# Kernel tuning notes

Hardware: AMD Instinct MI355X
Metric: run time of the kernel (lower is better)

The kernel has to match this reference:

```python
import jax, jax.numpy as jnp
import numpy as np

B, C, T_TEXT, T_FEAT = 32, 256, 512, 2048
DELTA = 0.1  # self.temperature


def setup_inputs() -> dict:
    key = jax.random.key(0)
    k1, k2 = jax.random.split(key)
    x = jax.random.normal(k1, (B, C, T_TEXT), dtype=jnp.float32)
    # token durations in frames, ~U[0, 8): avg ~4 frames/token -> T_FEAT ~ 2048
    w = jax.random.uniform(k2, (B, T_TEXT), dtype=jnp.float32) * 8.0
    x_mask = jnp.ones((B, T_TEXT), dtype=bool)
    y_mask = jnp.ones((B, T_FEAT), dtype=bool)
    return {"x": x, "w": w, "x_mask": x_mask, "y_mask": y_mask}


def reference(x, w, x_mask, y_mask):
    # Gaussian upsampling (arXiv 2010.04301) with fixed temperature DELTA.
    # x: (B, C, T_text), w: (B, T_text), x_mask: (B, T_text), y_mask: (B, T_feat)
    T_feats = y_mask.shape[-1]
    # frame time indices, zeroed where y_mask is False
    t = jnp.arange(T_feats, dtype=jnp.float32)[None, :] * y_mask.astype(jnp.float32)  # (B, T_feat)
    # Gaussian centers: cumulative duration minus half of own duration
    c = jnp.cumsum(w, axis=-1) - 0.5 * w  # (B, T_text)
    # energy: -delta * (t - c)^2  -> (B, T_feat, T_text)
    energy = -DELTA * (t[:, :, None] - c[:, None, :]) ** 2
    # mask out padded text tokens
    energy = jnp.where(x_mask[:, None, :], energy, -jnp.inf)
    p_attn = jax.nn.softmax(energy, axis=-1)  # (B, T_feat, T_text)
    # weighted sum over text tokens: (B, C, T_feat)
    out = jnp.einsum("btn,bcn->bct", p_attn, x)
    return out
```

## Files before the change

kernel.cpp:

```cpp
#include <hip/hip_runtime.h>
#include <hip/hip_bf16.h>

#define B_    32
#define C_    256
#define NT    512
#define TFEAT 2048
#define TT    32
#define UW    96
#define PRE   32
#define DELTA 0.1f
#define PSTR  104
#define TPB   4
#define NGRP  16

typedef __attribute__((ext_vector_type(4))) float f32x4;
typedef __attribute__((ext_vector_type(8))) unsigned short u16x8;
typedef __attribute__((ext_vector_type(8))) __bf16 bf16x8;

static __device__ inline unsigned short f2bfbits(float f) {
    __bf16 h = (__bf16)f;
    return __builtin_bit_cast(unsigned short, h);
}
static __device__ inline float bf2f(unsigned short h) {
    return __uint_as_float(((unsigned)h) << 16);
}

__global__ __launch_bounds__(256, 2) void fused_kernel(const float* __restrict__ x,
                                                       const float* __restrict__ w,
                                                       float* __restrict__ out) {
    __shared__ float cs[NT];
    __shared__ float wsum[8];
    __shared__ unsigned short Pt[2][TT][PSTR];
    __shared__ float Sinv[2][TT];
    __shared__ int sLO[TPB];

    int tid  = threadIdx.x;
    int bx   = blockIdx.x;
    int b    = bx & 31;
    int grp  = bx >> 5;
    int lane = tid & 63;
    int wv   = tid >> 6;

    float v0 = w[b * NT + tid];
    float v1 = w[b * NT + 256 + tid];
    float s0 = v0, s1 = v1;
#pragma unroll
    for (int off = 1; off < 64; off <<= 1) {
        float t0 = __shfl_up(s0, off);
        float t1 = __shfl_up(s1, off);
        if (lane >= off) { s0 += t0; s1 += t1; }
    }
    if (lane == 63) { wsum[wv] = s0; wsum[4 + wv] = s1; }
    __syncthreads();
    float pre0 = 0.f;
    float pre1 = wsum[0] + wsum[1] + wsum[2] + wsum[3];
#pragma unroll
    for (int i = 0; i < 4; ++i) if (i < wv) pre0 += wsum[i];
#pragma unroll
    for (int i = 0; i < 4; ++i) if (i < wv) pre1 += wsum[4 + i];
    cs[tid]       = pre0 + s0 - 0.5f * v0;
    cs[256 + tid] = pre1 + s1 - 0.5f * v1;
    __syncthreads();

    if (wv == 0) {
        int gid = lane >> 4;
        int k   = lane & 15;
        float ft = (float)((grp * TPB + gid) * TT);
        bool p = cs[32 * k + 31] < ft;
        unsigned long long m = __ballot(p);
        int K = __popcll((m >> (gid * 16)) & 0xFFFFull);
        int n;
        if (K >= 16) {
            n = NT;
        } else {
            int base = 32 * K;
            bool pa = cs[base + k] < ft;
            bool pb = cs[base + 16 + k] < ft;
            unsigned long long ma = __ballot(pa);
            unsigned long long mb = __ballot(pb);
            n = base + __popcll((ma >> (gid * 16)) & 0xFFFFull)
                     + __popcll((mb >> (gid * 16)) & 0xFFFFull);
        }
        if (k == 0) {
            int n1 = n < NT - 1 ? n : NT - 1;
            int n0 = n - 1 > 0 ? n - 1 : 0;
            int nstar = (fabsf(ft - cs[n0]) <= fabsf(ft - cs[n1])) ? n0 : n1;
            int L = (nstar - PRE) & ~3;
            if (L < 0) L = 0;
            if (L > NT - UW) L = NT - UW;
            sLO[gid] = L;
        }
    }
    __syncthreads();

    int g = tid >> 3, j = tid & 7;
    int arow = lane & 15, kg = lane >> 4;

    f32x4 areg[12][2];

    auto issue_A = [&](int it) {
        int LO = sLO[it];
        const float* xb = x + ((size_t)b * C_) * NT + LO + kg * 8;
#pragma unroll
        for (int m = 0; m < 4; ++m) {
            const float* xr = xb + (size_t)(wv * 64 + m * 16 + arow) * NT;
#pragma unroll
            for (int ks = 0; ks < 3; ++ks) {
                areg[m * 3 + ks][0] = *reinterpret_cast<const f32x4*>(xr + ks * 32);
                areg[m * 3 + ks][1] = *reinterpret_cast<const f32x4*>(xr + ks * 32 + 4);
            }
        }
    };

    auto softmax_tile = [&](int it, int bf) {
        int LO = sLO[it];
        float ft = (float)((grp * TPB + it) * TT + g);
        float e[12];
        float mx = -1e30f;
#pragma unroll
        for (int k = 0; k < 12; ++k) {
            float d = ft - cs[LO + j + 8 * k];
            e[k] = -DELTA * d * d;
            mx = fmaxf(mx, e[k]);
        }
        mx = fmaxf(mx, __shfl_xor(mx, 1));
        mx = fmaxf(mx, __shfl_xor(mx, 2));
        mx = fmaxf(mx, __shfl_xor(mx, 4));
        float sum = 0.f;
#pragma unroll
        for (int k = 0; k < 12; ++k) {
            unsigned short pbv = f2bfbits(__expf(e[k] - mx));
            sum += bf2f(pbv);
            Pt[bf][g][j + 8 * k] = pbv;
        }
        sum += __shfl_xor(sum, 1);
        sum += __shfl_xor(sum, 2);
        sum += __shfl_xor(sum, 4);
        if (j == 0) Sinv[bf][g] = 1.f / fmaxf(sum, 1e-30f);
    };

    issue_A(0);
    __builtin_amdgcn_sched_barrier(0);
    softmax_tile(0, 0);
    __syncthreads();

    for (int it = 0; it < TPB; ++it) {
        int bf = it & 1;

        bf16x8 bfrag[6];
#pragma unroll
        for (int nt2 = 0; nt2 < 2; ++nt2)
#pragma unroll
            for (int ks = 0; ks < 3; ++ks)
                bfrag[nt2 * 3 + ks] = __builtin_bit_cast(bf16x8,
                    *reinterpret_cast<const u16x8*>(
                        &Pt[bf][nt2 * 16 + arow][ks * 32 + kg * 8]));

        f32x4 acc[4][2];
#pragma unroll
        for (int m = 0; m < 4; ++m)
#pragma unroll
            for (int nt2 = 0; nt2 < 2; ++nt2)
                acc[m][nt2] = (f32x4){0.f, 0.f, 0.f, 0.f};

#pragma unroll
        for (int m = 0; m < 4; ++m) {
            bf16x8 af[3];
#pragma unroll
            for (int ks = 0; ks < 3; ++ks) {
                bf16x8 vv;
#pragma unroll
                for (int q = 0; q < 4; ++q) {
                    vv[q]     = (__bf16)areg[m * 3 + ks][0][q];
                    vv[q + 4] = (__bf16)areg[m * 3 + ks][1][q];
                }
                af[ks] = vv;
            }
#pragma unroll
            for (int nt2 = 0; nt2 < 2; ++nt2)
#pragma unroll
                for (int ks = 0; ks < 3; ++ks)
                    acc[m][nt2] = __builtin_amdgcn_mfma_f32_16x16x32_bf16(
                        af[ks], bfrag[nt2 * 3 + ks], acc[m][nt2], 0, 0, 0);
        }

        float si0 = Sinv[bf][arow];
        float si1 = Sinv[bf][16 + arow];

        if (it < TPB - 1) {
            issue_A(it + 1);
            __builtin_amdgcn_sched_barrier(0);
            softmax_tile(it + 1, bf ^ 1);
        }
        __syncthreads();

        int t0 = (grp * TPB + it) * TT;
        float* ob = out + ((size_t)b * C_) * TFEAT + t0;
        int orow = kg * 4;
#pragma unroll
        for (int m = 0; m < 4; ++m) {
            int c = wv * 64 + m * 16 + orow;
#pragma unroll
            for (int r = 0; r < 4; ++r) {
                __builtin_nontemporal_store(acc[m][0][r] * si0,
                    ob + (size_t)(c + r) * TFEAT + arow);
                __builtin_nontemporal_store(acc[m][1][r] * si1,
                    ob + (size_t)(c + r) * TFEAT + 16 + arow);
            }
        }
    }
}

extern "C" void kernel_launch(void* const* d_in, const int* in_sizes, int n_in,
                              void* d_out, int out_size, void* d_ws, size_t ws_size,
                              hipStream_t stream) {
    const float* x = (const float*)d_in[0];
    const float* w = (const float*)d_in[1];
    float* out = (float*)d_out;

    hipLaunchKernelGGL(fused_kernel, dim3(B_ * NGRP), dim3(256), 0, stream,
                       x, w, out);
}
```

Baseline: 35.81 us.

## Transpose output through LDS for vectorized stores and split work across more blocks

Swaps the MFMA operand order so each wave's accumulator tile can be scaled and transposed through a small LDS buffer, then written as coalesced 128-bit row stores. Previously each lane issued scalar nontemporal stores. It also halves the tiles per block and doubles the grid, removing the register prefetch of x and the double-buffered softmax pipeline. The goal is to cut store-transaction overhead on the large output write and raise parallelism. The cost is less overlap of loads with compute, an extra LDS round trip, and the loss of nontemporal store hints.

```diff
diff --git a/kernel.cpp b/kernel.cpp
--- a/kernel.cpp
+++ b/kernel.cpp
@@ -10,8 +10,9 @@
 #define PRE   32
 #define DELTA 0.1f
 #define PSTR  104
-#define TPB   4
-#define NGRP  16
+#define TPB   2
+#define NGRP  32
+#define TSTR  36
 
 typedef __attribute__((ext_vector_type(4))) float f32x4;
 typedef __attribute__((ext_vector_type(8))) unsigned short u16x8;
@@ -30,9 +31,10 @@
                                                        float* __restrict__ out) {
     __shared__ float cs[NT];
     __shared__ float wsum[8];
-    __shared__ unsigned short Pt[2][TT][PSTR];
-    __shared__ float Sinv[2][TT];
+    __shared__ unsigned short Pt[TT][PSTR];
+    __shared__ float Sinv[TT];
     __shared__ int sLO[TPB];
+    __shared__ float trans[4][16][TSTR];
 
     int tid  = threadIdx.x;
     int bx   = blockIdx.x;
@@ -65,149 +67,127 @@
     if (wv == 0) {
         int gid = lane >> 4;
         int k   = lane & 15;
-        float ft = (float)((grp * TPB + gid) * TT);
-        bool p = cs[32 * k + 31] < ft;
-        unsigned long long m = __ballot(p);
-        int K = __popcll((m >> (gid * 16)) & 0xFFFFull);
-        int n;
-        if (K >= 16) {
-            n = NT;
-        } else {
-            int base = 32 * K;
-            bool pa = cs[base + k] < ft;
-            bool pb = cs[base + 16 + k] < ft;
-            unsigned long long ma = __ballot(pa);
-            unsigned long long mb = __ballot(pb);
-            n = base + __popcll((ma >> (gid * 16)) & 0xFFFFull)
-                     + __popcll((mb >> (gid * 16)) & 0xFFFFull);
-        }
-        if (k == 0) {
-            int n1 = n < NT - 1 ? n : NT - 1;
-            int n0 = n - 1 > 0 ? n - 1 : 0;
-            int nstar = (fabsf(ft - cs[n0]) <= fabsf(ft - cs[n1])) ? n0 : n1;
-            int L = (nstar - PRE) & ~3;
-            if (L < 0) L = 0;
-            if (L > NT - UW) L = NT - UW;
-            sLO[gid] = L;
+        if (gid < TPB) {
+            float ft = (float)((grp * TPB + gid) * TT);
+            bool p = cs[32 * k + 31] < ft;
+            unsigned long long m = __ballot(p);
+            int K = __popcll((m >> (gid * 16)) & 0xFFFFull);
+            int n;
+            if (K >= 16) {
+                n = NT;
+            } else {
+                int base = 32 * K;
+                bool pa = cs[base + k] < ft;
+                bool pb = cs[base + 16 + k] < ft;
+                unsigned long long ma = __ballot(pa);
+                unsigned long long mb = __ballot(pb);
+                n = base + __popcll((ma >> (gid * 16)) & 0xFFFFull)
+                         + __popcll((mb >> (gid * 16)) & 0xFFFFull);
+            }
+            if (k == 0) {
+                int n1 = n < NT - 1 ? n : NT - 1;
+                int n0 = n - 1 > 0 ? n - 1 : 0;
+                int nstar = (fabsf(ft - cs[n0]) <= fabsf(ft - cs[n1])) ? n0 : n1;
+                int L = (nstar - PRE) & ~3;
+                if (L < 0) L = 0;
+                if (L > NT - UW) L = NT - UW;
+                sLO[gid] = L;
+            }
         }
     }
     __syncthreads();
 
     int g = tid >> 3, j = tid & 7;
     int arow = lane & 15, kg = lane >> 4;
-
-    f32x4 areg[12][2];
-
-    auto issue_A = [&](int it) {
+    int rr = lane >> 3, tq = lane & 7;
+
+    for (int it = 0; it < TPB; ++it) {
+        {
+            int LO = sLO[it];
+            float ft = (float)((grp * TPB + it) * TT + g);
+            float e[12];
+            float mx = -1e30f;
+#pragma unroll
+            for (int k = 0; k < 12; ++k) {
+                float d = ft - cs[LO + j + 8 * k];
+                e[k] = -DELTA * d * d;
+                mx = fmaxf(mx, e[k]);
+            }
+            mx = fmaxf(mx, __shfl_xor(mx, 1));
+            mx = fmaxf(mx, __shfl_xor(mx, 2));
+            mx = fmaxf(mx, __shfl_xor(mx, 4));
+            float sum = 0.f;
+#pragma unroll
+            for (int k = 0; k < 12; ++k) {
+                unsigned short pbv = f2bfbits(__expf(e[k] - mx));
+                sum += bf2f(pbv);
+                Pt[g][j + 8 * k] = pbv;
+            }
+            sum += __shfl_xor(sum, 1);
+            sum += __shfl_xor(sum, 2);
+            sum += __shfl_xor(sum, 4);
+            if (j == 0) Sinv[g] = 1.f / fmaxf(sum, 1e-30f);
+        }
+        __syncthreads();
+
         int LO = sLO[it];
+
+        bf16x8 pfrag[2][3];
+#pragma unroll
+        for (int tt = 0; tt < 2; ++tt)
+#pragma unroll
+            for (int ks = 0; ks < 3; ++ks)
+                pfrag[tt][ks] = __builtin_bit_cast(bf16x8,
+                    *reinterpret_cast<const u16x8*>(
+                        &Pt[tt * 16 + arow][ks * 32 + kg * 8]));
+
+        f32x4 acc[2][4];
+#pragma unroll
+        for (int tt = 0; tt < 2; ++tt)
+#pragma unroll
+            for (int m = 0; m < 4; ++m)
+                acc[tt][m] = (f32x4){0.f, 0.f, 0.f, 0.f};
+
         const float* xb = x + ((size_t)b * C_) * NT + LO + kg * 8;
 #pragma unroll
         for (int m = 0; m < 4; ++m) {
             const float* xr = xb + (size_t)(wv * 64 + m * 16 + arow) * NT;
+            bf16x8 xf[3];
 #pragma unroll
             for (int ks = 0; ks < 3; ++ks) {
-                areg[m * 3 + ks][0] = *reinterpret_cast<const f32x4*>(xr + ks * 32);
-                areg[m * 3 + ks][1] = *reinterpret_cast<const f32x4*>(xr + ks * 32 + 4);
-            }
-        }
-    };
-
-    auto softmax_tile = [&](int it, int bf) {
-        int LO = sLO[it];
-        float ft = (float)((grp * TPB + it) * TT + g);
-        float e[12];
-        float mx = -1e30f;
-#pragma unroll
-        for (int k = 0; k < 12; ++k) {
-            float d = ft - cs[LO + j + 8 * k];
-            e[k] = -DELTA * d * d;
-            mx = fmaxf(mx, e[k]);
-        }
-        mx = fmaxf(mx, __shfl_xor(mx, 1));
-        mx = fmaxf(mx, __shfl_xor(mx, 2));
-        mx = fmaxf(mx, __shfl_xor(mx, 4));
-        float sum = 0.f;
-#pragma unroll
-        for (int k = 0; k < 12; ++k) {
-            unsigned short pbv = f2bfbits(__expf(e[k] - mx));
-            sum += bf2f(pbv);
-            Pt[bf][g][j + 8 * k] = pbv;
-        }
-        sum += __shfl_xor(sum, 1);
-        sum += __shfl_xor(sum, 2);
-        sum += __shfl_xor(sum, 4);
-        if (j == 0) Sinv[bf][g] = 1.f / fmaxf(sum, 1e-30f);
-    };
-
-    issue_A(0);
-    __builtin_amdgcn_sched_barrier(0);
-    softmax_tile(0, 0);
-    __syncthreads();
-
-    for (int it = 0; it < TPB; ++it) {
-        int bf = it & 1;
-
-        bf16x8 bfrag[6];
-#pragma unroll
-        for (int nt2 = 0; nt2 < 2; ++nt2)
-#pragma unroll
-            for (int ks = 0; ks < 3; ++ks)
-                bfrag[nt2 * 3 + ks] = __builtin_bit_cast(bf16x8,
-                    *reinterpret_cast<const u16x8*>(
-                        &Pt[bf][nt2 * 16 + arow][ks * 32 + kg * 8]));
-
-        f32x4 acc[4][2];
-#pragma unroll
-        for (int m = 0; m < 4; ++m)
-#pragma unroll
-            for (int nt2 = 0; nt2 < 2; ++nt2)
-                acc[m][nt2] = (f32x4){0.f, 0.f, 0.f, 0.f};
-
+                f32x4 a0 = *reinterpret_cast<const f32x4*>(xr + ks * 32);
+                f32x4 a1 = *reinterpret_cast<const f32x4*>(xr + ks * 32 + 4);
+                bf16x8 vv;
+#pragma unroll
+                for (int q = 0; q < 4; ++q) {
+                    vv[q]     = (__bf16)a0[q];
+                    vv[q + 4] = (__bf16)a1[q];
+                }
+                xf[ks] = vv;
+            }
+#pragma unroll
+            for (int tt = 0; tt < 2; ++tt)
+#pragma unroll
+                for (int ks = 0; ks < 3; ++ks)
+                    acc[tt][m] = __builtin_amdgcn_mfma_f32_16x16x32_bf16(
+                        pfrag[tt][ks], xf[ks], acc[tt][m], 0, 0, 0);
+        }
+
+        int t0f = (grp * TPB + it) * TT;
+        float* ob = out + ((size_t)b * C_) * TFEAT + t0f;
+        f32x4 sv0 = *reinterpret_cast<const f32x4*>(&Sinv[kg * 4]);
+        f32x4 sv1 = *reinterpret_cast<const f32x4*>(&Sinv[16 + kg * 4]);
 #pragma unroll
         for (int m = 0; m < 4; ++m) {
-            bf16x8 af[3];
-#pragma unroll
-            for (int ks = 0; ks < 3; ++ks) {
-                bf16x8 vv;
-#pragma unroll
-                for (int q = 0; q < 4; ++q) {
-                    vv[q]     = (__bf16)areg[m * 3 + ks][0][q];
-                    vv[q + 4] = (__bf16)areg[m * 3 + ks][1][q];
-                }
-                af[ks] = vv;
-            }
-#pragma unroll
-            for (int nt2 = 0; nt2 < 2; ++nt2)
-#pragma unroll
-                for (int ks = 0; ks < 3; ++ks)
-                    acc[m][nt2] = __builtin_amdgcn_mfma_f32_16x16x32_bf16(
-                        af[ks], bfrag[nt2 * 3 + ks], acc[m][nt2], 0, 0, 0);
-        }
-
-        float si0 = Sinv[bf][arow];
-        float si1 = Sinv[bf][16 + arow];
-
-        if (it < TPB - 1) {
-            issue_A(it + 1);
-            __builtin_amdgcn_sched_barrier(0);
-            softmax_tile(it + 1, bf ^ 1);
+            *reinterpret_cast<f32x4*>(&trans[wv][arow][kg * 4])      = acc[0][m] * sv0;
+            *reinterpret_cast<f32x4*>(&trans[wv][arow][16 + kg * 4]) = acc[1][m] * sv1;
+            f32x4 o0 = *reinterpret_cast<const f32x4*>(&trans[wv][rr][tq * 4]);
+            f32x4 o1 = *reinterpret_cast<const f32x4*>(&trans[wv][8 + rr][tq * 4]);
+            int c0 = wv * 64 + m * 16;
+            *reinterpret_cast<f32x4*>(ob + (size_t)(c0 + rr) * TFEAT + tq * 4)     = o0;
+            *reinterpret_cast<f32x4*>(ob + (size_t)(c0 + 8 + rr) * TFEAT + tq * 4) = o1;
         }
         __syncthreads();
-
-        int t0 = (grp * TPB + it) * TT;
-        float* ob = out + ((size_t)b * C_) * TFEAT + t0;
-        int orow = kg * 4;
-#pragma unroll
-        for (int m = 0; m < 4; ++m) {
-            int c = wv * 64 + m * 16 + orow;
-#pragma unroll
-            for (int r = 0; r < 4; ++r) {
-                __builtin_nontemporal_store(acc[m][0][r] * si0,
-                    ob + (size_t)(c + r) * TFEAT + arow);
-                __builtin_nontemporal_store(acc[m][1][r] * si1,
-                    ob + (size_t)(c + r) * TFEAT + 16 + arow);
-            }
-        }
     }
 }
 
```

Result: faster. 34.86 us (-2.7%).
